# Kernel optimization log

Hardware: AMD Instinct MI355X
Metric: run time of the kernel (lower is better)

The kernel has to match this reference:

```python
import jax, jax.numpy as jnp
import numpy as np

N, D, NUM_CLASSES = 8192, 256, 512
DELTA = 1.0


def setup_inputs() -> dict:
    key = jax.random.key(0)
    k1, k2 = jax.random.split(key)
    queries = jax.random.normal(k1, (N, D), dtype=jnp.float32)
    targets = jax.random.randint(k2, (N,), 0, NUM_CLASSES, dtype=jnp.int64)
    return {"queries": queries, "targets": targets}


def _mine(queries, targets):
    # Pairwise squared L2 distances via gram expansion (avoids [N,N,D] intermediate).
    sq = jnp.sum(queries * queries, axis=-1)              # [N]
    dist = sq[:, None] + sq[None, :] - 2.0 * (queries @ queries.T)  # [N,N]
    same = targets[:, None] == targets[None, :]           # [N,N] bool
    diag = jnp.eye(dist.shape[0], dtype=bool)
    neg_inf = jnp.float32(-jnp.inf)
    # hardest positive: argmax over (distances * same_mask) with -inf diagonal
    pos_masked = jnp.where(diag, neg_inf, dist * same)
    pos_idx = jnp.argmax(pos_masked, axis=-1)
    # original: (-(distances * ~same, diag=-inf)).argmin == argmax of the masked matrix
    neg_masked = jnp.where(diag, neg_inf, dist * (~same))
    neg_idx = jnp.argmax(neg_masked, axis=-1)
    return pos_idx, neg_idx


def reference(queries, targets):
    pos_idx, neg_idx = _mine(queries, targets)
    pos = queries[pos_idx]                                # [N,D]
    neg = queries[neg_idx]                                # [N,D]
    d_pos = jnp.sum((queries - pos) ** 2, axis=-1, keepdims=True)  # [N,1]
    d_neg = jnp.sum((queries - neg) ** 2, axis=-1, keepdims=True)  # [N,1]
    loss = jax.nn.relu(DELTA - d_pos + d_neg)
    return jnp.mean(loss)
```

## Files before the change

### kernel.cpp

```cpp
#include <hip/hip_runtime.h>

#define N 8192
#define D 256
#define NB 64
#define NTILES (NB * (NB + 1) / 2)

typedef float f32x4 __attribute__((ext_vector_type(4)));
typedef long long i64;

__device__ __forceinline__ void gload16(const void* g, void* lds) {
    __builtin_amdgcn_global_load_lds(
        (const __attribute__((address_space(1))) void*)g,
        (__attribute__((address_space(3))) void*)lds, 16, 0, 0);
}


__global__ __launch_bounds__(256) void prep_kernel(const float* __restrict__ q,
                                                   unsigned char* __restrict__ q8,
                                                   float* __restrict__ sq,
                                                   unsigned* __restrict__ pos_key,
                                                   unsigned* __restrict__ neg_key,
                                                   float* __restrict__ out) {
    const int row = blockIdx.x * 4 + (threadIdx.x >> 6);
    const int lane = threadIdx.x & 63;
    if (threadIdx.x < 8) {
        const int r0 = blockIdx.x * 4 + (threadIdx.x >> 1);
        if (threadIdx.x & 1) neg_key[r0] = 0u; else pos_key[r0] = 0u;
    }
    if (blockIdx.x == 0 && threadIdx.x == 0) out[0] = 0.0f;
    const float4 v = ((const float4*)(q + row * D))[lane];
    int r = 0;
    r = __builtin_amdgcn_cvt_pk_fp8_f32(v.x, v.y, r, false);
    r = __builtin_amdgcn_cvt_pk_fp8_f32(v.z, v.w, r, true);
    ((int*)(q8 + (size_t)row * D))[lane] = r;
    float s = v.x * v.x + v.y * v.y + v.z * v.z + v.w * v.w;
    #pragma unroll
    for (int off = 32; off; off >>= 1) s += __shfl_down(s, off, 64);
    if (lane == 0) sq[row] = s;
}

__global__ __launch_bounds__(256, 3) void mine_kernel(
    const unsigned char* __restrict__ q8, const int* __restrict__ tgt,
    const float* __restrict__ sqv,
    unsigned* __restrict__ pos_key, unsigned* __restrict__ neg_key)
{
    __shared__ __align__(16) unsigned Msh[2 * 128 * 33];
    __shared__ float sqI[128], sqJ[128];
    __shared__ int   tgI[128], tgJ[128];
    char* const smem = (char*)Msh;

    int tt = blockIdx.x, bi = 0;
    while (tt >= NB - bi) { tt -= NB - bi; ++bi; }
    const int bj = bi + tt;
    const int i0 = bi * 128, j0 = bj * 128;
    const bool diag = (bi == bj);

    const int tid = threadIdx.x;
    const int w = tid >> 6, lane = tid & 63;
    const int quad = lane >> 4, lc = lane & 15;
    const int wy = w >> 1, wx = w & 1;

    if (tid < 128) { sqI[tid] = sqv[i0 + tid]; tgI[tid] = tgt[i0 + tid]; }
    else { const int c = tid - 128; sqJ[c] = sqv[j0 + c]; tgJ[c] = tgt[j0 + c]; }
    __syncthreads();

    float sqjn[4];
    #pragma unroll
    for (int nt = 0; nt < 4; ++nt) sqjn[nt] = sqJ[wx * 64 + nt * 16 + lc];
    f32x4 acc[4][4];
    #pragma unroll
    for (int mt = 0; mt < 4; ++mt) {
        const f32x4 si4 = *(const f32x4*)&sqI[wy * 64 + mt * 16 + quad * 4];
        #pragma unroll
        for (int nt = 0; nt < 4; ++nt)
            #pragma unroll
            for (int r = 0; r < 4; ++r)
                acc[mt][nt][r] = -0.5f * (si4[r] + sqjn[nt]);
    }

    for (int c = 0; c < D / 64; ++c) {
        const int dkb = c * 64;
        __syncthreads();
        #pragma unroll
        for (int it = 0; it < 2; ++it) {
            const int s = it * 256 + tid;
            const int r = s >> 2, bo = (s & 3) * 16;
            const int lbase = (it * 256 + w * 64) * 16;
            gload16(q8 + (size_t)(i0 + r) * D + dkb + bo, smem + lbase);
            if (!diag)
                gload16(q8 + (size_t)(j0 + r) * D + dkb + bo, smem + 8192 + lbase);
        }
        __syncthreads();

        const char* AP = smem;
        const char* BP = diag ? AP : smem + 8192;
        union { int4 v; i64 d[2]; } fb[4], fa;
        #pragma unroll
        for (int t = 0; t < 4; ++t)
            fb[t].v = *(const int4*)(BP + (wx * 64 + t * 16 + lc) * 64 + quad * 16);
        #pragma unroll
        for (int mt = 0; mt < 4; ++mt) {
            fa.v = *(const int4*)(AP + (wy * 64 + mt * 16 + lc) * 64 + quad * 16);
            #pragma unroll
            for (int nt = 0; nt < 4; ++nt) {
                acc[mt][nt] = __builtin_amdgcn_mfma_f32_16x16x32_fp8_fp8(
                    fa.d[0], fb[nt].d[0], acc[mt][nt], 0, 0, 0);
                acc[mt][nt] = __builtin_amdgcn_mfma_f32_16x16x32_fp8_fp8(
                    fa.d[1], fb[nt].d[1], acc[mt][nt], 0, 0, 0);
            }
        }
    }
    __syncthreads();

    unsigned* const mpos = Msh;
    unsigned* const mneg = Msh + 128 * 33;

    int tj[4]; unsigned jc[4], jpk[4], jnk[4];
    #pragma unroll
    for (int nt = 0; nt < 4; ++nt) {
        const int cl = wx * 64 + nt * 16 + lc;
        tj[nt] = tgJ[cl];
        jc[nt] = 0x1FFFu - (unsigned)(j0 + cl);
        jpk[nt] = 0u; jnk[nt] = 0u;
    }

    #pragma unroll
    for (int mt = 0; mt < 4; ++mt) {
        const int rbase = wy * 64 + mt * 16 + quad * 4;
        const int4 ti4 = *(const int4*)&tgI[rbase];
        #pragma unroll
        for (int r = 0; r < 4; ++r) {
            const int sr = rbase + r;
            const unsigned rk = 0x1FFFu - (unsigned)(i0 + sr);
            const int ti = ((const int*)&ti4)[r];
            unsigned bpk = 0u, bnk = 0u;
            #pragma unroll
            for (int nt = 0; nt < 4; ++nt) {
                const int cl = wx * 64 + nt * 16 + lc;
                const float dist = fmaxf(-2.0f * acc[mt][nt][r], 0.0f);
                const unsigned db = __float_as_uint(dist) & 0xFFFFE000u;
                const bool same = (ti == tj[nt]);
                const bool dia = diag && (sr == cl);
                const unsigned pb_ = dia ? 0u : (same ? db : 0u);
                const unsigned nb_ = dia ? 0u : (same ? 0u : db);
                bpk = max(bpk, dia ? 0u : (pb_ | jc[nt]));
                bnk = max(bnk, dia ? 0u : (nb_ | jc[nt]));
                jpk[nt] = max(jpk[nt], dia ? 0u : (pb_ | rk));
                jnk[nt] = max(jnk[nt], dia ? 0u : (nb_ | rk));
            }
            mpos[sr * 33 + wx * 16 + lc] = bpk;
            mneg[sr * 33 + wx * 16 + lc] = bnk;
        }
    }
    __syncthreads();

    {
        const int sr = tid & 127;
        const unsigned* m = (tid < 128) ? &mpos[sr * 33] : &mneg[sr * 33];
        unsigned best = 0u;
        #pragma unroll
        for (int k = 0; k < 32; ++k) best = max(best, m[k]);
        unsigned* gk = (tid < 128) ? pos_key : neg_key;
        atomicMax(&gk[i0 + sr], best);
    }

    if (!diag) {
        #pragma unroll
        for (int nt = 0; nt < 4; ++nt) {
            unsigned pk = jpk[nt], nk = jnk[nt];
            #pragma unroll
            for (int off = 16; off < 64; off <<= 1) {
                pk = max(pk, (unsigned)__shfl_xor((int)pk, off, 64));
                nk = max(nk, (unsigned)__shfl_xor((int)nk, off, 64));
            }
            if (quad == 0) {
                const int gcol = j0 + wx * 64 + nt * 16 + lc;
                atomicMax(&pos_key[gcol], pk);
                atomicMax(&neg_key[gcol], nk);
            }
        }
    }
}

__global__ __launch_bounds__(256) void final_kernel(
    const float* __restrict__ q, const unsigned* __restrict__ pos_key,
    const unsigned* __restrict__ neg_key, float* __restrict__ out)
{
    __shared__ float red[4];
    const int wv = threadIdx.x >> 6, lane = threadIdx.x & 63;
    float wsum = 0.0f;
    for (int rr = 0; rr < 32; ++rr) {
        const int row = (blockIdx.x * 4 + wv) * 32 + rr;
        const int bpi = 0x1FFF - (int)(pos_key[row] & 0x1FFFu);
        const int bni = 0x1FFF - (int)(neg_key[row] & 0x1FFFu);
        const float4 qi = ((const float4*)(q + row * D))[lane];
        const float4 qp = ((const float4*)(q + (size_t)bpi * D))[lane];
        const float4 qn = ((const float4*)(q + (size_t)bni * D))[lane];
        float dx, dp = 0.0f, dn = 0.0f;
        dx = qi.x - qp.x; dp += dx * dx;
        dx = qi.y - qp.y; dp += dx * dx;
        dx = qi.z - qp.z; dp += dx * dx;
        dx = qi.w - qp.w; dp += dx * dx;
        dx = qi.x - qn.x; dn += dx * dx;
        dx = qi.y - qn.y; dn += dx * dx;
        dx = qi.z - qn.z; dn += dx * dx;
        dx = qi.w - qn.w; dn += dx * dx;
        #pragma unroll
        for (int off = 32; off; off >>= 1) {
            dp += __shfl_down(dp, off, 64);
            dn += __shfl_down(dn, off, 64);
        }
        if (lane == 0) wsum += fmaxf(0.0f, (1.0f - dp) + dn);
    }
    if (lane == 0) red[wv] = wsum;
    __syncthreads();
    if (threadIdx.x == 0)
        atomicAdd(out, (red[0] + red[1] + red[2] + red[3]) * (1.0f / N));
}

extern "C" void kernel_launch(void* const* d_in, const int* in_sizes, int n_in,
                              void* d_out, int out_size, void* d_ws, size_t ws_size,
                              hipStream_t stream) {
    const float* q = (const float*)d_in[0];
    const int* tgt = (const int*)d_in[1];
    float* out = (float*)d_out;

    unsigned* pos_key = (unsigned*)d_ws;
    unsigned* neg_key = pos_key + N;
    unsigned char* q8 = (unsigned char*)(neg_key + N);
    float* sqv = (float*)(q8 + (size_t)N * D);

    prep_kernel<<<dim3(N / 4), dim3(256), 0, stream>>>(q, q8, sqv, pos_key, neg_key, out);
    mine_kernel<<<dim3(NTILES), dim3(256), 0, stream>>>(q8, tgt, sqv, pos_key, neg_key);
    final_kernel<<<dim3(64), dim3(256), 0, stream>>>(q, pos_key, neg_key, out);
}
```

Measured before the change: 106.2 us.

## Preload all K chunks into LDS upfront and streamline the mining epilogue

Instead of looping over four 64-byte K chunks with a load and two barriers each, every block now issues all fp8 tile loads for the full D at once into a 64 KB LDS buffer. One barrier then precedes the MFMA loop, which removes the per-chunk barrier stalls and puts more loads in flight. The key-mining epilogue is split into off-diagonal and diagonal paths. It uses a cheaper selection (ki - pi_) for the negative key, and the diagonal path drops the unused column reductions. The larger LDS footprint, 64 KB plus small arrays per block, likely cuts blocks per CU below the launch-bounds hint of 3. Diagonal self-entries now keep their index bits rather than being zeroed.

```diff
diff --git a/kernel.cpp b/kernel.cpp
--- a/kernel.cpp
+++ b/kernel.cpp
@@ -44,10 +44,9 @@
     const float* __restrict__ sqv,
     unsigned* __restrict__ pos_key, unsigned* __restrict__ neg_key)
 {
-    __shared__ __align__(16) unsigned Msh[2 * 128 * 33];
+    __shared__ __align__(16) char smem[65536];
     __shared__ float sqI[128], sqJ[128];
     __shared__ int   tgI[128], tgJ[128];
-    char* const smem = (char*)Msh;
 
     int tt = blockIdx.x, bi = 0;
     while (tt >= NB - bi) { tt -= NB - bi; ++bi; }
@@ -62,6 +61,20 @@
 
     if (tid < 128) { sqI[tid] = sqv[i0 + tid]; tgI[tid] = tgt[i0 + tid]; }
     else { const int c = tid - 128; sqJ[c] = sqv[j0 + c]; tgJ[c] = tgt[j0 + c]; }
+
+    #pragma unroll
+    for (int c = 0; c < 4; ++c) {
+        #pragma unroll
+        for (int it = 0; it < 2; ++it) {
+            const int s = it * 256 + tid;
+            const int r = s >> 2, bo = (s & 3) * 16;
+            const int lbase = c * 8192 + (it * 256 + w * 64) * 16;
+            gload16(q8 + (size_t)(i0 + r) * D + c * 64 + bo, smem + lbase);
+            if (!diag)
+                gload16(q8 + (size_t)(j0 + r) * D + c * 64 + bo,
+                        smem + 32768 + lbase);
+        }
+    }
     __syncthreads();
 
     float sqjn[4];
@@ -78,22 +91,9 @@
                 acc[mt][nt][r] = -0.5f * (si4[r] + sqjn[nt]);
     }
 
-    for (int c = 0; c < D / 64; ++c) {
-        const int dkb = c * 64;
-        __syncthreads();
-        #pragma unroll
-        for (int it = 0; it < 2; ++it) {
-            const int s = it * 256 + tid;
-            const int r = s >> 2, bo = (s & 3) * 16;
-            const int lbase = (it * 256 + w * 64) * 16;
-            gload16(q8 + (size_t)(i0 + r) * D + dkb + bo, smem + lbase);
-            if (!diag)
-                gload16(q8 + (size_t)(j0 + r) * D + dkb + bo, smem + 8192 + lbase);
-        }
-        __syncthreads();
-
-        const char* AP = smem;
-        const char* BP = diag ? AP : smem + 8192;
+    for (int c = 0; c < 4; ++c) {
+        const char* AP = smem + c * 8192;
+        const char* BP = diag ? AP : smem + 32768 + c * 8192;
         union { int4 v; i64 d[2]; } fb[4], fa;
         #pragma unroll
         for (int t = 0; t < 4; ++t)
@@ -112,8 +112,8 @@
     }
     __syncthreads();
 
-    unsigned* const mpos = Msh;
-    unsigned* const mneg = Msh + 128 * 33;
+    unsigned* const mpos = (unsigned*)smem;
+    unsigned* const mneg = mpos + 128 * 33;
 
     int tj[4]; unsigned jc[4], jpk[4], jnk[4];
     #pragma unroll
@@ -134,19 +134,34 @@
             const unsigned rk = 0x1FFFu - (unsigned)(i0 + sr);
             const int ti = ((const int*)&ti4)[r];
             unsigned bpk = 0u, bnk = 0u;
-            #pragma unroll
-            for (int nt = 0; nt < 4; ++nt) {
-                const int cl = wx * 64 + nt * 16 + lc;
-                const float dist = fmaxf(-2.0f * acc[mt][nt][r], 0.0f);
-                const unsigned db = __float_as_uint(dist) & 0xFFFFE000u;
-                const bool same = (ti == tj[nt]);
-                const bool dia = diag && (sr == cl);
-                const unsigned pb_ = dia ? 0u : (same ? db : 0u);
-                const unsigned nb_ = dia ? 0u : (same ? 0u : db);
-                bpk = max(bpk, dia ? 0u : (pb_ | jc[nt]));
-                bnk = max(bnk, dia ? 0u : (nb_ | jc[nt]));
-                jpk[nt] = max(jpk[nt], dia ? 0u : (pb_ | rk));
-                jnk[nt] = max(jnk[nt], dia ? 0u : (nb_ | rk));
+            if (!diag) {
+                #pragma unroll
+                for (int nt = 0; nt < 4; ++nt) {
+                    const float dist = fmaxf(-2.0f * acc[mt][nt][r], 0.0f);
+                    const unsigned db = __float_as_uint(dist) & 0xFFFFE000u;
+                    const bool same = (ti == tj[nt]);
+                    const unsigned ki = db | jc[nt];
+                    const unsigned pi_ = same ? ki : 0u;
+                    bpk = max(bpk, pi_);
+                    bnk = max(bnk, ki - pi_);
+                    const unsigned kj = db | rk;
+                    const unsigned pj_ = same ? kj : 0u;
+                    jpk[nt] = max(jpk[nt], pj_);
+                    jnk[nt] = max(jnk[nt], kj - pj_);
+                }
+            } else {
+                #pragma unroll
+                for (int nt = 0; nt < 4; ++nt) {
+                    const int cl = wx * 64 + nt * 16 + lc;
+                    const float dist = fmaxf(-2.0f * acc[mt][nt][r], 0.0f);
+                    const unsigned db = (sr == cl) ? 0u
+                        : (__float_as_uint(dist) & 0xFFFFE000u);
+                    const bool same = (ti == tj[nt]);
+                    const unsigned ki = db | jc[nt];
+                    const unsigned pi_ = same ? ki : 0u;
+                    bpk = max(bpk, pi_);
+                    bnk = max(bnk, ki - pi_);
+                }
             }
             mpos[sr * 33 + wx * 16 + lc] = bpk;
             mneg[sr * 33 + wx * 16 + lc] = bnk;
```

Measured after the change: 112.2 us. 5.7% more time.

## Fuse final loss reduction into mining kernel via global completion flags

Applied to the files above, without the earlier changes.

Removes the separate final kernel launch. Every mining block publishes a completion flag, and the last 64 blocks spin until all tiles are done before computing the hinge loss and atomically accumulating the mean. This saves a launch and its gap, but the flags are never reset, so they stay set from a previous call and later calls may read incomplete keys. Blocks spinning while others are still unscheduled also risk deadlock.

```diff
diff --git a/kernel.cpp b/kernel.cpp
--- a/kernel.cpp
+++ b/kernel.cpp
@@ -4,6 +4,7 @@
 #define D 256
 #define NB 64
 #define NTILES (NB * (NB + 1) / 2)
+#define MAGIC 0x13579BDFu
 
 typedef float f32x4 __attribute__((ext_vector_type(4)));
 typedef long long i64;
@@ -41,8 +42,9 @@
 
 __global__ __launch_bounds__(256, 3) void mine_kernel(
     const unsigned char* __restrict__ q8, const int* __restrict__ tgt,
-    const float* __restrict__ sqv,
-    unsigned* __restrict__ pos_key, unsigned* __restrict__ neg_key)
+    const float* __restrict__ sqv, const float* __restrict__ q,
+    unsigned* __restrict__ pos_key, unsigned* __restrict__ neg_key,
+    unsigned* __restrict__ dflags, float* __restrict__ out)
 {
     __shared__ __align__(16) unsigned Msh[2 * 128 * 33];
     __shared__ float sqI[128], sqJ[128];
@@ -180,42 +182,51 @@
             }
         }
     }
-}
-
-__global__ __launch_bounds__(256) void final_kernel(
-    const float* __restrict__ q, const unsigned* __restrict__ pos_key,
-    const unsigned* __restrict__ neg_key, float* __restrict__ out)
-{
-    __shared__ float red[4];
-    const int wv = threadIdx.x >> 6, lane = threadIdx.x & 63;
-    float wsum = 0.0f;
-    for (int rr = 0; rr < 32; ++rr) {
-        const int row = (blockIdx.x * 4 + wv) * 32 + rr;
-        const int bpi = 0x1FFF - (int)(pos_key[row] & 0x1FFFu);
-        const int bni = 0x1FFF - (int)(neg_key[row] & 0x1FFFu);
-        const float4 qi = ((const float4*)(q + row * D))[lane];
-        const float4 qp = ((const float4*)(q + (size_t)bpi * D))[lane];
-        const float4 qn = ((const float4*)(q + (size_t)bni * D))[lane];
-        float dx, dp = 0.0f, dn = 0.0f;
-        dx = qi.x - qp.x; dp += dx * dx;
-        dx = qi.y - qp.y; dp += dx * dx;
-        dx = qi.z - qp.z; dp += dx * dx;
-        dx = qi.w - qp.w; dp += dx * dx;
-        dx = qi.x - qn.x; dn += dx * dx;
-        dx = qi.y - qn.y; dn += dx * dx;
-        dx = qi.z - qn.z; dn += dx * dx;
-        dx = qi.w - qn.w; dn += dx * dx;
-        #pragma unroll
-        for (int off = 32; off; off >>= 1) {
-            dp += __shfl_down(dp, off, 64);
-            dn += __shfl_down(dn, off, 64);
-        }
-        if (lane == 0) wsum += fmaxf(0.0f, (1.0f - dp) + dn);
-    }
-    if (lane == 0) red[wv] = wsum;
-    __syncthreads();
-    if (threadIdx.x == 0)
-        atomicAdd(out, (red[0] + red[1] + red[2] + red[3]) * (1.0f / N));
+
+    __threadfence();
+    if (tid == 0)
+        __hip_atomic_store(&dflags[blockIdx.x], MAGIC,
+                           __ATOMIC_RELEASE, __HIP_MEMORY_SCOPE_AGENT);
+
+    if (blockIdx.x >= NTILES - 64) {
+        for (int i = tid; i < NTILES; i += 256)
+            while (__hip_atomic_load(&dflags[i], __ATOMIC_ACQUIRE,
+                                     __HIP_MEMORY_SCOPE_AGENT) != MAGIC)
+                __builtin_amdgcn_s_sleep(2);
+        __syncthreads();
+
+        __shared__ float red[4];
+        const int fb = blockIdx.x - (NTILES - 64);
+        const int wv = tid >> 6;
+        float wsum = 0.0f;
+        for (int rr = 0; rr < 32; ++rr) {
+            const int row = (fb * 4 + wv) * 32 + rr;
+            const int bpi = 0x1FFF - (int)(pos_key[row] & 0x1FFFu);
+            const int bni = 0x1FFF - (int)(neg_key[row] & 0x1FFFu);
+            const float4 qi = ((const float4*)(q + row * D))[lane];
+            const float4 qp = ((const float4*)(q + (size_t)bpi * D))[lane];
+            const float4 qn = ((const float4*)(q + (size_t)bni * D))[lane];
+            float dx, dp = 0.0f, dn = 0.0f;
+            dx = qi.x - qp.x; dp += dx * dx;
+            dx = qi.y - qp.y; dp += dx * dx;
+            dx = qi.z - qp.z; dp += dx * dx;
+            dx = qi.w - qp.w; dp += dx * dx;
+            dx = qi.x - qn.x; dn += dx * dx;
+            dx = qi.y - qn.y; dn += dx * dx;
+            dx = qi.z - qn.z; dn += dx * dx;
+            dx = qi.w - qn.w; dn += dx * dx;
+            #pragma unroll
+            for (int off = 32; off; off >>= 1) {
+                dp += __shfl_down(dp, off, 64);
+                dn += __shfl_down(dn, off, 64);
+            }
+            if (lane == 0) wsum += fmaxf(0.0f, (1.0f - dp) + dn);
+        }
+        if (lane == 0) red[wv] = wsum;
+        __syncthreads();
+        if (tid == 0)
+            atomicAdd(out, (red[0] + red[1] + red[2] + red[3]) * (1.0f / N));
+    }
 }
 
 extern "C" void kernel_launch(void* const* d_in, const int* in_sizes, int n_in,
@@ -229,8 +240,9 @@
     unsigned* neg_key = pos_key + N;
     unsigned char* q8 = (unsigned char*)(neg_key + N);
     float* sqv = (float*)(q8 + (size_t)N * D);
+    unsigned* dflags = (unsigned*)(sqv + N);
 
     prep_kernel<<<dim3(N / 4), dim3(256), 0, stream>>>(q, q8, sqv, pos_key, neg_key, out);
-    mine_kernel<<<dim3(NTILES), dim3(256), 0, stream>>>(q8, tgt, sqv, pos_key, neg_key);
-    final_kernel<<<dim3(64), dim3(256), 0, stream>>>(q, pos_key, neg_key, out);
-}
+    mine_kernel<<<dim3(NTILES), dim3(256), 0, stream>>>(
+        q8, tgt, sqv, q, pos_key, neg_key, dflags, out);
+}
```

After: 242.5 us. 2.28x slower.
